# Optimization experiments

Measured on AMD Instinct MI355X. Metric: run time of the kernel, lower is better.

## Reference

```python
import jax, jax.numpy as jnp
import numpy as np

NEG_SLOPE = 0.2
EPS = 1e-16

N_NODES = 50000
N_EDGES = 1600000
IN_CH = 256
HID = 16
HEADS = 2


def setup_inputs() -> dict:
    key = jax.random.key(0)
    ks = jax.random.split(key, 12)
    s = lambda k, shape, scale=0.1: jax.random.normal(k, shape, dtype=jnp.float32) * scale
    x = jax.random.normal(ks[0], (N_NODES, IN_CH), dtype=jnp.float32)
    edge_index = jax.random.randint(ks[1], (2, N_EDGES), 0, N_NODES, dtype=jnp.int64)
    return {
        "x": x,
        "edge_index": edge_index,
        "W1": s(ks[2], (IN_CH, HEADS * HID)),
        "att_src1": s(ks[3], (HEADS, HID)),
        "att_dst1": s(ks[4], (HEADS, HID)),
        "b1": jnp.zeros((HEADS * HID,), jnp.float32),
        "W2": s(ks[5], (HEADS * HID, HID)),
        "att_src2": s(ks[6], (1, HID)),
        "att_dst2": s(ks[7], (1, HID)),
        "b2": jnp.zeros((HID,), jnp.float32),
        "Wm1": s(ks[8], (2 * HID, HID)),
        "bm1": jnp.zeros((HID,), jnp.float32),
        "Wm2": s(ks[9], (HID, 1)),
        "bm2": jnp.zeros((1,), jnp.float32),
    }


def gat_conv(x, src, dst, W, att_src, att_dst, bias, heads, out_ch, concat):
    # x: [N, F] -> h: [N, H, C]
    n = x.shape[0]
    h = (x @ W).reshape(n, heads, out_ch)
    # per-node attention logits [N, H]
    a_src = jnp.sum(h * att_src, axis=-1)
    a_dst = jnp.sum(h * att_dst, axis=-1)
    # per-edge logits: message j (src) -> i (dst); softmax grouped by dst
    e = a_src[src] + a_dst[dst]                      # [E, H]
    e = jax.nn.leaky_relu(e, NEG_SLOPE)
    e_max = jax.ops.segment_max(e, dst, num_segments=n)
    e_exp = jnp.exp(e - e_max[dst])
    denom = jax.ops.segment_sum(e_exp, dst, num_segments=n)
    alpha = e_exp / (denom[dst] + EPS)               # [E, H]
    msg = alpha[:, :, None] * h[src]                 # [E, H, C]
    out = jax.ops.segment_sum(msg, dst, num_segments=n)  # [N, H, C]
    out = out.reshape(n, heads * out_ch) if concat else out.mean(axis=1)
    return out + bias


def reference(x, edge_index, W1, att_src1, att_dst1, b1,
              W2, att_src2, att_dst2, b2, Wm1, bm1, Wm2, bm2):
    src, dst = edge_index[0], edge_index[1]
    # eval mode: feature/attention dropout are identity
    h = gat_conv(x, src, dst, W1, att_src1, att_dst1, b1, HEADS, HID, concat=True)
    h = jax.nn.elu(h)
    h = gat_conv(h, src, dst, W2, att_src2, att_dst2, b2, 1, HID, concat=False)
    # edge MLP on gathered (src, dst) node pairs
    ef = jnp.concatenate([h[src], h[dst]], axis=-1)  # [E, 2*HID]
    ef = jax.nn.relu(ef @ Wm1 + bm1)
    flow = (ef @ Wm2 + bm2).squeeze(-1)              # [E]
    return jax.nn.relu(flow)
```

## Files before the change

### kernel.cpp

```cpp
#include <hip/hip_runtime.h>
#include <hip/hip_bf16.h>
#include <hip/hip_fp16.h>

#define N_NODES 50000
#define N_EDGES 1600000
#define IN_CH 256
#define NEG_SLOPE 0.2f
#define EPS_F 1e-16f
#define CNT_PAD 16
#define CAP 128
#define NBK 196
#define CAPB 10240
#define PCHUNK 3125
#define KTILE 64
#define XS_PITCH (KTILE + 4)

__device__ __forceinline__ float lrelu(float x) {
    return x > 0.f ? x : NEG_SLOPE * x;
}

__device__ __forceinline__ float2 h2f(unsigned int w) {
    __half2 h;
    *reinterpret_cast<unsigned int*>(&h) = w;
    return __half22float2(h);
}

__device__ __forceinline__ unsigned int f2h2(float a, float b) {
    __half2 h = __floats2half2_rn(a, b);
    return *reinterpret_cast<unsigned int*>(&h);
}

__device__ __forceinline__ int detect_i64(const int* __restrict__ ei) {
    const int lane = threadIdx.x & 63;
    const unsigned long long b = __ballot(ei[2 * lane + 1] != 0);
    return b == 0ull ? 1 : 0;
}

__device__ __forceinline__ int ld_src(const int* ei, int f, int e) {
    return f ? ei[2 * (size_t)e] : ei[e];
}
__device__ __forceinline__ int ld_dst(const int* ei, int f, int e) {
    return f ? ei[2 * (size_t)N_EDGES + 2 * (size_t)e]
             : ei[(size_t)N_EDGES + e];
}

__global__ __launch_bounds__(1024) void k_part(const int* __restrict__ ei,
                                               int* __restrict__ gcnt,
                                               int2* __restrict__ bseg)
{
    __shared__ int hist[NBK];
    __shared__ int cur[NBK];
    const int t = threadIdx.x;
    const int f = detect_i64(ei);
    for (int j = t; j < NBK; j += 1024) hist[j] = 0;
    __syncthreads();
    const int e0 = blockIdx.x * PCHUNK;
    const int e1 = min(e0 + PCHUNK, N_EDGES);
    for (int e = e0 + t; e < e1; e += 1024)
        atomicAdd(&hist[ld_dst(ei, f, e) >> 8], 1);
    __syncthreads();
    for (int j = t; j < NBK; j += 1024)
        cur[j] = j * CAPB + atomicAdd(&gcnt[j], hist[j]);
    __syncthreads();
    for (int e = e0 + t; e < e1; e += 1024) {
        const int s = ld_src(ei, f, e);
        const int d = ld_dst(ei, f, e);
        const int bk = d >> 8;
        const int pos = atomicAdd(&cur[bk], 1);
        if (pos - bk * CAPB < CAPB) bseg[pos] = make_int2(s, d);
    }
}

__global__ __launch_bounds__(1024) void k_sub(const int* __restrict__ gcnt,
                                              const int2* __restrict__ bseg,
                                              int* __restrict__ cnt,
                                              int* __restrict__ csr_src)
{
    __shared__ int cur[256];
    const int b = blockIdx.x;
    const int t = threadIdx.x;
    if (t < 256) cur[t] = 0;
    __syncthreads();
    const int count = min(gcnt[b], CAPB);
    const int2* seg = bseg + (size_t)b * CAPB;
    for (int i = t; i < count; i += 1024) {
        const int2 e = seg[i];
        const int slot = atomicAdd(&cur[e.y & 255], 1);
        if (slot < CAP) csr_src[((size_t)e.y << 7) + slot] = e.x;
    }
    __syncthreads();
    if (t < 256) {
        const int n = b * 256 + t;
        if (n < N_NODES) cnt[(size_t)n * CNT_PAD] = min(cur[t], CAP);
    }
}

__global__ __launch_bounds__(256) void k1_gemm1(
    const float* __restrict__ x, const float* __restrict__ W1,
    const float* __restrict__ att_src1, const float* __restrict__ att_dst1,
    __half* __restrict__ h1, float* __restrict__ a_src1, float* __restrict__ a_dst1)
{
    __shared__ float w1s[IN_CH * 32];
    __shared__ float xs[64 * XS_PITCH];
    __shared__ float attss[32], attds[32];
    const int t = threadIdx.x;
    for (int i = t; i < IN_CH * 32; i += 256) w1s[i] = W1[i];
    if (t < 32) { attss[t] = att_src1[t]; attds[t] = att_dst1[t]; }
    const int row0 = blockIdx.x * 64;
    const int colq = t & 7, c4 = colq * 4;
    const int rp = t >> 3;
    const int r0 = rp * 2, r1 = r0 + 1;
    float4 a0 = make_float4(0.f, 0.f, 0.f, 0.f);
    float4 a1 = make_float4(0.f, 0.f, 0.f, 0.f);
    for (int kb = 0; kb < IN_CH; kb += KTILE) {
        __syncthreads();
        #pragma unroll
        for (int i = 0; i < 4; ++i) {
            const int idx = t + 256 * i;
            const int r = idx >> 4, p = idx & 15;
            const int row = row0 + r;
            float4 vv = make_float4(0.f, 0.f, 0.f, 0.f);
            if (row < N_NODES)
                vv = *(const float4*)(x + (size_t)row * IN_CH + kb + p * 4);
            *(float4*)(&xs[r * XS_PITCH + p * 4]) = vv;
        }
        __syncthreads();
        #pragma unroll 8
        for (int kt = 0; kt < KTILE; ++kt) {
            const float xv0 = xs[r0 * XS_PITCH + kt];
            const float xv1 = xs[r1 * XS_PITCH + kt];
            const float4 wv = *(const float4*)(&w1s[(kb + kt) * 32 + c4]);
            a0.x += xv0 * wv.x; a0.y += xv0 * wv.y;
            a0.z += xv0 * wv.z; a0.w += xv0 * wv.w;
            a1.x += xv1 * wv.x; a1.y += xv1 * wv.y;
            a1.z += xv1 * wv.z; a1.w += xv1 * wv.w;
        }
    }
    const int row_a = row0 + r0, row_b = row0 + r1;
    if (row_a < N_NODES) {
        uint2 p; p.x = f2h2(a0.x, a0.y); p.y = f2h2(a0.z, a0.w);
        *(uint2*)(h1 + (size_t)row_a * 32 + c4) = p;
    }
    if (row_b < N_NODES) {
        uint2 p; p.x = f2h2(a1.x, a1.y); p.y = f2h2(a1.z, a1.w);
        *(uint2*)(h1 + (size_t)row_b * 32 + c4) = p;
    }
    float sa0 = a0.x * attss[c4] + a0.y * attss[c4 + 1]
              + a0.z * attss[c4 + 2] + a0.w * attss[c4 + 3];
    float sd0 = a0.x * attds[c4] + a0.y * attds[c4 + 1]
              + a0.z * attds[c4 + 2] + a0.w * attds[c4 + 3];
    float sa1 = a1.x * attss[c4] + a1.y * attss[c4 + 1]
              + a1.z * attss[c4 + 2] + a1.w * attss[c4 + 3];
    float sd1 = a1.x * attds[c4] + a1.y * attds[c4 + 1]
              + a1.z * attds[c4 + 2] + a1.w * attds[c4 + 3];
    sa0 += __shfl_xor(sa0, 1); sa0 += __shfl_xor(sa0, 2);
    sd0 += __shfl_xor(sd0, 1); sd0 += __shfl_xor(sd0, 2);
    sa1 += __shfl_xor(sa1, 1); sa1 += __shfl_xor(sa1, 2);
    sd1 += __shfl_xor(sd1, 1); sd1 += __shfl_xor(sd1, 2);
    const int head = colq >> 2;
    if ((colq & 3) == 0) {
        if (row_a < N_NODES) {
            a_src1[row_a * 2 + head] = sa0;
            a_dst1[row_a * 2 + head] = sd0;
        }
        if (row_b < N_NODES) {
            a_src1[row_b * 2 + head] = sa1;
            a_dst1[row_b * 2 + head] = sd1;
        }
    }
}

__global__ __launch_bounds__(256) void k_agg1f(
    const int* __restrict__ cnt, const int* __restrict__ csr_src,
    const float* __restrict__ a_src1, const float* __restrict__ a_dst1,
    const __half* __restrict__ h1,
    const float* __restrict__ b1, const float* __restrict__ W2,
    const float* __restrict__ att_src2, const float* __restrict__ att_dst2,
    __half* __restrict__ h2, float* __restrict__ a_src2, float* __restrict__ a_dst2)
{
    __shared__ float w2s[32 * 16];
    __shared__ float b1s[32], as2[16], ad2[16];
    __shared__ float act_s[4][32];
    const int t = threadIdx.x;
    for (int i = t; i < 512; i += 256) w2s[i] = W2[i];
    if (t < 32) b1s[t] = b1[t];
    if (t < 16) { as2[t] = att_src2[t]; ad2[t] = att_dst2[t]; }

    const int wid = (blockIdx.x * 256 + t) >> 6;
    const int lane = t & 63;
    const int wv = t >> 6;
    const int active = (wid < N_NODES);
    const int len = active ? min(cnt[(size_t)wid * CNT_PAD], CAP) : 0;
    const int beg = wid << 7, end = beg + len;
    float2 ad = make_float2(0.f, 0.f);
    if (active) ad = *(const float2*)(a_dst1 + 2 * (size_t)wid);
    const int slot = lane >> 4, chp = lane & 15;
    const int head = chp >> 3;
    const float adh = head ? ad.y : ad.x;
    const int rep = ((chp & 7) == 0);
    const unsigned int* __restrict__ h1u = (const unsigned int*)h1;
    float accx = 0.f, accy = 0.f, sw = 0.f;
    int i = beg + slot;
    for (; i + 28 < end; i += 32) {
        int s[8]; float a[8]; unsigned int hw[8]; float w[8];
        #pragma unroll
        for (int j = 0; j < 8; ++j) s[j] = csr_src[i + 4 * j];
        #pragma unroll
        for (int j = 0; j < 8; ++j) a[j] = a_src1[2 * (size_t)s[j] + head];
        #pragma unroll
        for (int j = 0; j < 8; ++j) hw[j] = h1u[(size_t)s[j] * 16 + chp];
        #pragma unroll
        for (int j = 0; j < 8; ++j) w[j] = __expf(lrelu(a[j] + adh));
        float wsum = 0.f;
        #pragma unroll
        for (int j = 0; j < 8; ++j) {
            const float2 hf = h2f(hw[j]);
            wsum += w[j];
            accx += w[j] * hf.x; accy += w[j] * hf.y;
        }
        if (rep) sw += wsum;
    }
    for (; i + 12 < end; i += 16) {
        int s[4]; float a[4]; unsigned int hw[4]; float w[4];
        #pragma unroll
        for (int j = 0; j < 4; ++j) s[j] = csr_src[i + 4 * j];
        #pragma unroll
        for (int j = 0; j < 4; ++j) a[j] = a_src1[2 * (size_t)s[j] + head];
        #pragma unroll
        for (int j = 0; j < 4; ++j) hw[j] = h1u[(size_t)s[j] * 16 + chp];
        #pragma unroll
        for (int j = 0; j < 4; ++j) w[j] = __expf(lrelu(a[j] + adh));
        float wsum = 0.f;
        #pragma unroll
        for (int j = 0; j < 4; ++j) {
            const float2 hf = h2f(hw[j]);
            wsum += w[j];
            accx += w[j] * hf.x; accy += w[j] * hf.y;
        }
        if (rep) sw += wsum;
    }
    for (; i < end; i += 4) {
        const int s = csr_src[i];
        const float w = __expf(lrelu(a_src1[2 * (size_t)s + head] + adh));
        if (rep) sw += w;
        const float2 hf = h2f(h1u[(size_t)s * 16 + chp]);
        accx += w * hf.x; accy += w * hf.y;
    }
    sw += __shfl_xor(sw, 16); sw += __shfl_xor(sw, 32);
    const float swh = __shfl(sw, head << 3);
    accx += __shfl_xor(accx, 16); accx += __shfl_xor(accx, 32);
    accy += __shfl_xor(accy, 16); accy += __shfl_xor(accy, 32);
    const float inv = 1.f / (swh + EPS_F);
    if (lane < 16) {
        float ax = accx * inv + b1s[2 * chp];
        float ay = accy * inv + b1s[2 * chp + 1];
        ax = ax > 0.f ? ax : expm1f(ax);
        ay = ay > 0.f ? ay : expm1f(ay);
        act_s[wv][2 * chp] = ax;
        act_s[wv][2 * chp + 1] = ay;
    }
    __syncthreads();
    const int j = lane & 15;
    float acc2 = 0.f;
    #pragma unroll
    for (int k = 0; k < 32; ++k) acc2 += act_s[wv][k] * w2s[k * 16 + j];
    if (lane < 16 && active) h2[(size_t)wid * 16 + j] = __float2half(acc2);
    float sa = acc2 * as2[j], sd = acc2 * ad2[j];
    sa += __shfl_xor(sa, 1); sa += __shfl_xor(sa, 2);
    sa += __shfl_xor(sa, 4); sa += __shfl_xor(sa, 8);
    sd += __shfl_xor(sd, 1); sd += __shfl_xor(sd, 2);
    sd += __shfl_xor(sd, 4); sd += __shfl_xor(sd, 8);
    if (lane == 0 && active) { a_src2[wid] = sa; a_dst2[wid] = sd; }
}

__global__ __launch_bounds__(256) void k_agg2f(
    const int* __restrict__ cnt, const int* __restrict__ csr_src,
    const float* __restrict__ a_src2, const float* __restrict__ a_dst2,
    const __half* __restrict__ h2,
    const float* __restrict__ b2, const float* __restrict__ Wm1,
    const float* __restrict__ bm1,
    __half* __restrict__ u, __half* __restrict__ v)
{
    __shared__ float wa[16 * 16], wb[16 * 16];
    __shared__ float b2s[16], bm1s[16];
    __shared__ float act_s[4][16];
    const int t = threadIdx.x;
    if (t < 256) { wa[t] = Wm1[t]; wb[t] = Wm1[256 + t]; }
    if (t < 16) { b2s[t] = b2[t]; bm1s[t] = bm1[t]; }

    const int wid = (blockIdx.x * 256 + t) >> 6;
    const int lane = t & 63;
    const int wv = t >> 6;
    const int active = (wid < N_NODES);
    const int len = active ? min(cnt[(size_t)wid * CNT_PAD], CAP) : 0;
    const int beg = wid << 7, end = beg + len;
    const float ad = active ? a_dst2[wid] : 0.f;
    const int slot = lane >> 3, chp = lane & 7;
    const int rep = (chp == 0);
    const unsigned int* __restrict__ h2u = (const unsigned int*)h2;
    float accx = 0.f, accy = 0.f, sw = 0.f;
    int i = beg + slot;
    for (; i + 24 < end; i += 32) {
        int s[4]; float a[4]; unsigned int hw[4]; float w[4];
        #pragma unroll
        for (int j = 0; j < 4; ++j) s[j] = csr_src[i + 8 * j];
        #pragma unroll
        for (int j = 0; j < 4; ++j) a[j] = a_src2[s[j]];
        #pragma unroll
        for (int j = 0; j < 4; ++j) hw[j] = h2u[(size_t)s[j] * 8 + chp];
        #pragma unroll
        for (int j = 0; j < 4; ++j) w[j] = __expf(lrelu(a[j] + ad));
        float wsum = 0.f;
        #pragma unroll
        for (int j = 0; j < 4; ++j) {
            const float2 hf = h2f(hw[j]);
            wsum += w[j];
            accx += w[j] * hf.x; accy += w[j] * hf.y;
        }
        if (rep) sw += wsum;
    }
    for (; i < end; i += 8) {
        const int s = csr_src[i];
        const float w = __expf(lrelu(a_src2[s] + ad));
        if (rep) sw += w;
        const float2 hf = h2f(h2u[(size_t)s * 8 + chp]);
        accx += w * hf.x; accy += w * hf.y;
    }
    sw += __shfl_xor(sw, 8); sw += __shfl_xor(sw, 16); sw += __shfl_xor(sw, 32);
    const float swt = __shfl(sw, 0);
    accx += __shfl_xor(accx, 8); accx += __shfl_xor(accx, 16); accx += __shfl_xor(accx, 32);
    accy += __shfl_xor(accy, 8); accy += __shfl_xor(accy, 16); accy += __shfl_xor(accy, 32);
    const float inv = 1.f / (swt + EPS_F);
    if (lane < 8) {
        float2 o;
        o.x = accx * inv + b2s[2 * chp];
        o.y = accy * inv + b2s[2 * chp + 1];
        *(float2*)(&act_s[wv][2 * chp]) = o;
    }
    __syncthreads();
    const int c = lane & 15;
    float su = bm1s[c], sv = 0.f;
    #pragma unroll
    for (int k = 0; k < 16; ++k) {
        const float a = act_s[wv][k];
        su += a * wa[k * 16 + c];
        sv += a * wb[k * 16 + c];
    }
    if (lane < 16 && active) {
        u[(size_t)wid * 16 + c] = __float2half(su);
        v[(size_t)wid * 16 + c] = __float2half(sv);
    }
}

__global__ __launch_bounds__(256) void k7_lite(
    const int* __restrict__ ei,
    const __half* __restrict__ u, const __half* __restrict__ v,
    const float* __restrict__ Wm2, const float* __restrict__ bm2,
    float* __restrict__ out)
{
    __shared__ float wm2s[16];
    __shared__ float bm2s;
    const int t = threadIdx.x;
    const int f = detect_i64(ei);
    if (t < 16) wm2s[t] = Wm2[t];
    if (t == 0) bm2s = bm2[0];
    __syncthreads();
    const int e = blockIdx.x * 256 + t;
    if (e >= N_EDGES) return;
    const int s = ld_src(ei, f, e);
    const int d = ld_dst(ei, f, e);
    const uint4* up = (const uint4*)(u + (size_t)s * 16);
    const uint4* vp = (const uint4*)(v + (size_t)d * 16);
    const uint4 ua = up[0], ub = up[1];
    const uint4 va = vp[0], vb = vp[1];
    float fl = bm2s;
    unsigned int uw[8] = {ua.x, ua.y, ua.z, ua.w, ub.x, ub.y, ub.z, ub.w};
    unsigned int vw[8] = {va.x, va.y, va.z, va.w, vb.x, vb.y, vb.z, vb.w};
    #pragma unroll
    for (int i = 0; i < 8; ++i) {
        const float2 a = h2f(uw[i]);
        const float2 b = h2f(vw[i]);
        fl += fmaxf(a.x + b.x, 0.f) * wm2s[2 * i];
        fl += fmaxf(a.y + b.y, 0.f) * wm2s[2 * i + 1];
    }
    out[e] = fmaxf(fl, 0.f);
}

extern "C" void kernel_launch(void* const* d_in, const int* in_sizes, int n_in,
                              void* d_out, int out_size, void* d_ws, size_t ws_size,
                              hipStream_t stream)
{
    const float* x        = (const float*)d_in[0];
    const int*   ei       = (const int*)d_in[1];
    const float* W1       = (const float*)d_in[2];
    const float* att_src1 = (const float*)d_in[3];
    const float* att_dst1 = (const float*)d_in[4];
    const float* b1       = (const float*)d_in[5];
    const float* W2       = (const float*)d_in[6];
    const float* att_src2 = (const float*)d_in[7];
    const float* att_dst2 = (const float*)d_in[8];
    const float* b2       = (const float*)d_in[9];
    const float* Wm1      = (const float*)d_in[10];
    const float* bm1      = (const float*)d_in[11];
    const float* Wm2      = (const float*)d_in[12];
    const float* bm2      = (const float*)d_in[13];

    float* ws = (float*)d_ws;
    size_t off = 0;
    __half* h1 = (__half*)(ws + off); off += 16 * (size_t)N_NODES;
    float* a_src1 = ws + off; off += 2  * (size_t)N_NODES;
    float* a_dst1 = ws + off; off += 2  * (size_t)N_NODES;
    float* out1_dead = ws + off; off += 32 * (size_t)N_NODES;
    __half* h2 = (__half*)(ws + off); off += 16 * (size_t)N_NODES;
    float* a_src2 = ws + off; off += 1  * (size_t)N_NODES;
    float* a_dst2 = ws + off; off += 1  * (size_t)N_NODES;
    float* out2_dead = ws + off; off += 16 * (size_t)N_NODES;
    __half* u = (__half*)(ws + off); off += 8 * (size_t)N_NODES;
    __half* v = (__half*)(ws + off); off += 8 * (size_t)N_NODES;
    int* cnt     = (int*)(ws + off); off += (size_t)N_NODES * CNT_PAD;
    int* csr_src = (int*)(ws + off); off += (size_t)N_NODES * CAP;
    int* gcnt    = (int*)(ws + off); off += 256;
    int* flag    = (int*)(ws + off); off += 64;
    (void)out1_dead; (void)out2_dead; (void)flag;
    int2* bseg = (int2*)ws;

    hipMemsetAsync(gcnt, 0, 256 * sizeof(int), stream);
    k_part<<<(N_EDGES + PCHUNK - 1) / PCHUNK, 1024, 0, stream>>>(ei, gcnt, bseg);
    k_sub<<<NBK, 1024, 0, stream>>>(gcnt, bseg, cnt, csr_src);

    k1_gemm1<<<(N_NODES + 63) / 64, 256, 0, stream>>>(
        x, W1, att_src1, att_dst1, h1, a_src1, a_dst1);
    k_agg1f<<<(N_NODES + 3) / 4, 256, 0, stream>>>(
        cnt, csr_src, a_src1, a_dst1, h1, b1, W2, att_src2, att_dst2,
        h2, a_src2, a_dst2);
    k_agg2f<<<(N_NODES + 3) / 4, 256, 0, stream>>>(
        cnt, csr_src, a_src2, a_dst2, h2, b2, Wm1, bm1, u, v);
    k7_lite<<<(N_EDGES + 255) / 256, 256, 0, stream>>>(
        ei, u, v, Wm2, bm2, (float*)d_out);
}
```

Measured before the change: 259.3 us.

## Compute edge weights once per edge and broadcast via shuffles in GAT aggregation

The two neighbor-aggregation kernels now have each lane load one CSR source index and compute one attention weight, then broadcast indices and weights to the channel lanes with wave shuffles. Before, every channel lane reloaded csr_src and a_src and recomputed exp redundantly. The partition kernel also keeps the src/dst values it loaded in registers between the histogram and scatter passes, so edge_index is read once instead of twice. This adds many shuffle instructions and loses the multi-edge unrolled loads that were in flight together, which may reduce memory-level parallelism for the feature gathers.

```diff
diff --git a/kernel.cpp b/kernel.cpp
--- a/kernel.cpp
+++ b/kernel.cpp
@@ -56,18 +56,26 @@
     __syncthreads();
     const int e0 = blockIdx.x * PCHUNK;
     const int e1 = min(e0 + PCHUNK, N_EDGES);
-    for (int e = e0 + t; e < e1; e += 1024)
-        atomicAdd(&hist[ld_dst(ei, f, e) >> 8], 1);
+    int es[4], ed[4];
+    int ne = 0;
+    #pragma unroll
+    for (int q = 0; q < 4; ++q) {
+        const int e = e0 + t + 1024 * q;
+        if (e < e1) {
+            es[ne] = ld_src(ei, f, e);
+            ed[ne] = ld_dst(ei, f, e);
+            ++ne;
+        }
+    }
+    for (int q = 0; q < ne; ++q) atomicAdd(&hist[ed[q] >> 8], 1);
     __syncthreads();
     for (int j = t; j < NBK; j += 1024)
         cur[j] = j * CAPB + atomicAdd(&gcnt[j], hist[j]);
     __syncthreads();
-    for (int e = e0 + t; e < e1; e += 1024) {
-        const int s = ld_src(ei, f, e);
-        const int d = ld_dst(ei, f, e);
-        const int bk = d >> 8;
+    for (int q = 0; q < ne; ++q) {
+        const int bk = ed[q] >> 8;
         const int pos = atomicAdd(&cur[bk], 1);
-        if (pos - bk * CAPB < CAPB) bseg[pos] = make_int2(s, d);
+        if (pos - bk * CAPB < CAPB) bseg[pos] = make_int2(es[q], ed[q]);
     }
 }
 
@@ -194,60 +202,36 @@
     const int beg = wid << 7, end = beg + len;
     float2 ad = make_float2(0.f, 0.f);
     if (active) ad = *(const float2*)(a_dst1 + 2 * (size_t)wid);
+
+    const int e_off = lane >> 1;
+    const int hh = lane & 1;
+    const float adh_a = hh ? ad.y : ad.x;
     const int slot = lane >> 4, chp = lane & 15;
     const int head = chp >> 3;
-    const float adh = head ? ad.y : ad.x;
-    const int rep = ((chp & 7) == 0);
+
     const unsigned int* __restrict__ h1u = (const unsigned int*)h1;
     float accx = 0.f, accy = 0.f, sw = 0.f;
-    int i = beg + slot;
-    for (; i + 28 < end; i += 32) {
-        int s[8]; float a[8]; unsigned int hw[8]; float w[8];
-        #pragma unroll
-        for (int j = 0; j < 8; ++j) s[j] = csr_src[i + 4 * j];
-        #pragma unroll
-        for (int j = 0; j < 8; ++j) a[j] = a_src1[2 * (size_t)s[j] + head];
-        #pragma unroll
-        for (int j = 0; j < 8; ++j) hw[j] = h1u[(size_t)s[j] * 16 + chp];
-        #pragma unroll
-        for (int j = 0; j < 8; ++j) w[j] = __expf(lrelu(a[j] + adh));
-        float wsum = 0.f;
+    for (int i0 = beg; i0 < end; i0 += 32) {
+        const int el = i0 + e_off;
+        int s_a = 0; float w_a = 0.f;
+        if (el < end) {
+            s_a = csr_src[el];
+            const float av = a_src1[2 * (size_t)s_a + hh];
+            w_a = __expf(lrelu(av + adh_a));
+        }
+        sw += w_a;
         #pragma unroll
         for (int j = 0; j < 8; ++j) {
-            const float2 hf = h2f(hw[j]);
-            wsum += w[j];
-            accx += w[j] * hf.x; accy += w[j] * hf.y;
-        }
-        if (rep) sw += wsum;
-    }
-    for (; i + 12 < end; i += 16) {
-        int s[4]; float a[4]; unsigned int hw[4]; float w[4];
-        #pragma unroll
-        for (int j = 0; j < 4; ++j) s[j] = csr_src[i + 4 * j];
-        #pragma unroll
-        for (int j = 0; j < 4; ++j) a[j] = a_src1[2 * (size_t)s[j] + head];
-        #pragma unroll
-        for (int j = 0; j < 4; ++j) hw[j] = h1u[(size_t)s[j] * 16 + chp];
-        #pragma unroll
-        for (int j = 0; j < 4; ++j) w[j] = __expf(lrelu(a[j] + adh));
-        float wsum = 0.f;
-        #pragma unroll
-        for (int j = 0; j < 4; ++j) {
-            const float2 hf = h2f(hw[j]);
-            wsum += w[j];
-            accx += w[j] * hf.x; accy += w[j] * hf.y;
-        }
-        if (rep) sw += wsum;
-    }
-    for (; i < end; i += 4) {
-        const int s = csr_src[i];
-        const float w = __expf(lrelu(a_src1[2 * (size_t)s + head] + adh));
-        if (rep) sw += w;
-        const float2 hf = h2f(h1u[(size_t)s * 16 + chp]);
-        accx += w * hf.x; accy += w * hf.y;
-    }
-    sw += __shfl_xor(sw, 16); sw += __shfl_xor(sw, 32);
-    const float swh = __shfl(sw, head << 3);
+            const int sl = (slot * 8 + j) * 2;
+            const int s_j = __shfl(s_a, sl);
+            const float w_j = __shfl(w_a, sl + head);
+            const float2 hf = h2f(h1u[(size_t)s_j * 16 + chp]);
+            accx += w_j * hf.x; accy += w_j * hf.y;
+        }
+    }
+    sw += __shfl_xor(sw, 2); sw += __shfl_xor(sw, 4);
+    sw += __shfl_xor(sw, 8); sw += __shfl_xor(sw, 16); sw += __shfl_xor(sw, 32);
+    const float swh = __shfl(sw, head);
     accx += __shfl_xor(accx, 16); accx += __shfl_xor(accx, 32);
     accy += __shfl_xor(accy, 16); accy += __shfl_xor(accy, 32);
     const float inv = 1.f / (swh + EPS_F);
@@ -296,41 +280,30 @@
     const int beg = wid << 7, end = beg + len;
     const float ad = active ? a_dst2[wid] : 0.f;
     const int slot = lane >> 3, chp = lane & 7;
-    const int rep = (chp == 0);
     const unsigned int* __restrict__ h2u = (const unsigned int*)h2;
     float accx = 0.f, accy = 0.f, sw = 0.f;
-    int i = beg + slot;
-    for (; i + 24 < end; i += 32) {
-        int s[4]; float a[4]; unsigned int hw[4]; float w[4];
+    for (int i0 = beg; i0 < end; i0 += 64) {
+        const int el = i0 + lane;
+        int s_a = 0; float w_a = 0.f;
+        if (el < end) {
+            s_a = csr_src[el];
+            w_a = __expf(lrelu(a_src2[s_a] + ad));
+        }
+        sw += w_a;
         #pragma unroll
-        for (int j = 0; j < 4; ++j) s[j] = csr_src[i + 8 * j];
-        #pragma unroll
-        for (int j = 0; j < 4; ++j) a[j] = a_src2[s[j]];
-        #pragma unroll
-        for (int j = 0; j < 4; ++j) hw[j] = h2u[(size_t)s[j] * 8 + chp];
-        #pragma unroll
-        for (int j = 0; j < 4; ++j) w[j] = __expf(lrelu(a[j] + ad));
-        float wsum = 0.f;
-        #pragma unroll
-        for (int j = 0; j < 4; ++j) {
-            const float2 hf = h2f(hw[j]);
-            wsum += w[j];
-            accx += w[j] * hf.x; accy += w[j] * hf.y;
-        }
-        if (rep) sw += wsum;
-    }
-    for (; i < end; i += 8) {
-        const int s = csr_src[i];
-        const float w = __expf(lrelu(a_src2[s] + ad));
-        if (rep) sw += w;
-        const float2 hf = h2f(h2u[(size_t)s * 8 + chp]);
-        accx += w * hf.x; accy += w * hf.y;
-    }
+        for (int j = 0; j < 8; ++j) {
+            const int sl = slot * 8 + j;
+            const int s_j = __shfl(s_a, sl);
+            const float w_j = __shfl(w_a, sl);
+            const float2 hf = h2f(h2u[(size_t)s_j * 8 + chp]);
+            accx += w_j * hf.x; accy += w_j * hf.y;
+        }
+    }
+    sw += __shfl_xor(sw, 1); sw += __shfl_xor(sw, 2); sw += __shfl_xor(sw, 4);
     sw += __shfl_xor(sw, 8); sw += __shfl_xor(sw, 16); sw += __shfl_xor(sw, 32);
-    const float swt = __shfl(sw, 0);
     accx += __shfl_xor(accx, 8); accx += __shfl_xor(accx, 16); accx += __shfl_xor(accx, 32);
     accy += __shfl_xor(accy, 8); accy += __shfl_xor(accy, 16); accy += __shfl_xor(accy, 32);
-    const float inv = 1.f / (swt + EPS_F);
+    const float inv = 1.f / (sw + EPS_F);
     if (lane < 8) {
         float2 o;
         o.x = accx * inv + b2s[2 * chp];
```

Result: no change. 259.1 us (-0.1%).

## Replace two-pass bucketed CSR build with direct global-atomic slot insertion

Applied to the files above, without the earlier changes.

Removes the two-kernel partition (block histogram into 196 buckets, then a per-bucket sub-sort through LDS atomics) and builds the padded CSR in one kernel. That kernel does a global atomicAdd on each destination's padded counter and writes the source into that slot. This drops one launch and the intermediate bseg round trip. In exchange it issues 1.6M scattered global atomics, and a memset now has to clear the padded count array. Slot order inside a node becomes nondeterministic, which can change float summation order.

```diff
diff --git a/kernel.cpp b/kernel.cpp
--- a/kernel.cpp
+++ b/kernel.cpp
@@ -9,9 +9,6 @@
 #define EPS_F 1e-16f
 #define CNT_PAD 16
 #define CAP 128
-#define NBK 196
-#define CAPB 10240
-#define PCHUNK 3125
 #define KTILE 64
 #define XS_PITCH (KTILE + 4)
 
@@ -44,55 +41,17 @@
              : ei[(size_t)N_EDGES + e];
 }
 
-__global__ __launch_bounds__(1024) void k_part(const int* __restrict__ ei,
-                                               int* __restrict__ gcnt,
-                                               int2* __restrict__ bseg)
-{
-    __shared__ int hist[NBK];
-    __shared__ int cur[NBK];
-    const int t = threadIdx.x;
+__global__ __launch_bounds__(256) void k_build(const int* __restrict__ ei,
+                                               int* __restrict__ cnt,
+                                               int* __restrict__ csr_src)
+{
     const int f = detect_i64(ei);
-    for (int j = t; j < NBK; j += 1024) hist[j] = 0;
-    __syncthreads();
-    const int e0 = blockIdx.x * PCHUNK;
-    const int e1 = min(e0 + PCHUNK, N_EDGES);
-    for (int e = e0 + t; e < e1; e += 1024)
-        atomicAdd(&hist[ld_dst(ei, f, e) >> 8], 1);
-    __syncthreads();
-    for (int j = t; j < NBK; j += 1024)
-        cur[j] = j * CAPB + atomicAdd(&gcnt[j], hist[j]);
-    __syncthreads();
-    for (int e = e0 + t; e < e1; e += 1024) {
-        const int s = ld_src(ei, f, e);
-        const int d = ld_dst(ei, f, e);
-        const int bk = d >> 8;
-        const int pos = atomicAdd(&cur[bk], 1);
-        if (pos - bk * CAPB < CAPB) bseg[pos] = make_int2(s, d);
-    }
-}
-
-__global__ __launch_bounds__(1024) void k_sub(const int* __restrict__ gcnt,
-                                              const int2* __restrict__ bseg,
-                                              int* __restrict__ cnt,
-                                              int* __restrict__ csr_src)
-{
-    __shared__ int cur[256];
-    const int b = blockIdx.x;
-    const int t = threadIdx.x;
-    if (t < 256) cur[t] = 0;
-    __syncthreads();
-    const int count = min(gcnt[b], CAPB);
-    const int2* seg = bseg + (size_t)b * CAPB;
-    for (int i = t; i < count; i += 1024) {
-        const int2 e = seg[i];
-        const int slot = atomicAdd(&cur[e.y & 255], 1);
-        if (slot < CAP) csr_src[((size_t)e.y << 7) + slot] = e.x;
-    }
-    __syncthreads();
-    if (t < 256) {
-        const int n = b * 256 + t;
-        if (n < N_NODES) cnt[(size_t)n * CNT_PAD] = min(cur[t], CAP);
-    }
+    const int e = blockIdx.x * 256 + threadIdx.x;
+    if (e >= N_EDGES) return;
+    const int s = ld_src(ei, f, e);
+    const int d = ld_dst(ei, f, e);
+    const int pos = atomicAdd(&cnt[(size_t)d * CNT_PAD], 1);
+    if (pos < CAP) csr_src[((size_t)d << 7) + pos] = s;
 }
 
 __global__ __launch_bounds__(256) void k1_gemm1(
@@ -410,23 +369,19 @@
     __half* h1 = (__half*)(ws + off); off += 16 * (size_t)N_NODES;
     float* a_src1 = ws + off; off += 2  * (size_t)N_NODES;
     float* a_dst1 = ws + off; off += 2  * (size_t)N_NODES;
-    float* out1_dead = ws + off; off += 32 * (size_t)N_NODES;
+    float* spare1 = ws + off; off += 32 * (size_t)N_NODES;
     __half* h2 = (__half*)(ws + off); off += 16 * (size_t)N_NODES;
     float* a_src2 = ws + off; off += 1  * (size_t)N_NODES;
     float* a_dst2 = ws + off; off += 1  * (size_t)N_NODES;
-    float* out2_dead = ws + off; off += 16 * (size_t)N_NODES;
+    float* spare2 = ws + off; off += 16 * (size_t)N_NODES;
     __half* u = (__half*)(ws + off); off += 8 * (size_t)N_NODES;
     __half* v = (__half*)(ws + off); off += 8 * (size_t)N_NODES;
     int* cnt     = (int*)(ws + off); off += (size_t)N_NODES * CNT_PAD;
     int* csr_src = (int*)(ws + off); off += (size_t)N_NODES * CAP;
-    int* gcnt    = (int*)(ws + off); off += 256;
-    int* flag    = (int*)(ws + off); off += 64;
-    (void)out1_dead; (void)out2_dead; (void)flag;
-    int2* bseg = (int2*)ws;
-
-    hipMemsetAsync(gcnt, 0, 256 * sizeof(int), stream);
-    k_part<<<(N_EDGES + PCHUNK - 1) / PCHUNK, 1024, 0, stream>>>(ei, gcnt, bseg);
-    k_sub<<<NBK, 1024, 0, stream>>>(gcnt, bseg, cnt, csr_src);
+    (void)spare1; (void)spare2;
+
+    hipMemsetAsync(cnt, 0, (size_t)N_NODES * CNT_PAD * sizeof(int), stream);
+    k_build<<<(N_EDGES + 255) / 256, 256, 0, stream>>>(ei, cnt, csr_src);
 
     k1_gemm1<<<(N_NODES + 63) / 64, 256, 0, stream>>>(
         x, W1, att_src1, att_dst1, h1, a_src1, a_dst1);
```

Result: slower. 340.9 us (+31.5%).

## Precompute layer-1 attention weights into CSR records during bucket scatter

Applied to the files above, without the earlier changes.

Reorders the launches so the first GEMM runs before CSR construction. The sub-bucket scatter can then compute both heads' exp(leaky_relu) layer-1 attention weights and store them next to the source index in 16-byte records. The layer-1 aggregation reads these records in place of gathering a_src1 and evaluating exp per edge per lane. The partition kernel also keeps its src/dst loads in registers so edge_index is read once, not twice. In exchange CSR storage grows fourfold, so the layer-2 aggregation reads 16-byte records just to get the index, and k_sub now does random gathers of a_src1.

```diff
diff --git a/kernel.cpp b/kernel.cpp
--- a/kernel.cpp
+++ b/kernel.cpp
@@ -56,25 +56,35 @@
     __syncthreads();
     const int e0 = blockIdx.x * PCHUNK;
     const int e1 = min(e0 + PCHUNK, N_EDGES);
-    for (int e = e0 + t; e < e1; e += 1024)
-        atomicAdd(&hist[ld_dst(ei, f, e) >> 8], 1);
+    int es[4], ed[4];
+    int ne = 0;
+    #pragma unroll
+    for (int q = 0; q < 4; ++q) {
+        const int e = e0 + t + 1024 * q;
+        if (e < e1) {
+            es[ne] = ld_src(ei, f, e);
+            ed[ne] = ld_dst(ei, f, e);
+            ++ne;
+        }
+    }
+    for (int q = 0; q < ne; ++q) atomicAdd(&hist[ed[q] >> 8], 1);
     __syncthreads();
     for (int j = t; j < NBK; j += 1024)
         cur[j] = j * CAPB + atomicAdd(&gcnt[j], hist[j]);
     __syncthreads();
-    for (int e = e0 + t; e < e1; e += 1024) {
-        const int s = ld_src(ei, f, e);
-        const int d = ld_dst(ei, f, e);
-        const int bk = d >> 8;
+    for (int q = 0; q < ne; ++q) {
+        const int bk = ed[q] >> 8;
         const int pos = atomicAdd(&cur[bk], 1);
-        if (pos - bk * CAPB < CAPB) bseg[pos] = make_int2(s, d);
+        if (pos - bk * CAPB < CAPB) bseg[pos] = make_int2(es[q], ed[q]);
     }
 }
 
 __global__ __launch_bounds__(1024) void k_sub(const int* __restrict__ gcnt,
                                               const int2* __restrict__ bseg,
+                                              const float* __restrict__ a_src1,
+                                              const float* __restrict__ a_dst1,
                                               int* __restrict__ cnt,
-                                              int* __restrict__ csr_src)
+                                              int4* __restrict__ csr_rec)
 {
     __shared__ int cur[256];
     const int b = blockIdx.x;
@@ -86,7 +96,18 @@
     for (int i = t; i < count; i += 1024) {
         const int2 e = seg[i];
         const int slot = atomicAdd(&cur[e.y & 255], 1);
-        if (slot < CAP) csr_src[((size_t)e.y << 7) + slot] = e.x;
+        if (slot < CAP) {
+            const float2 as = *(const float2*)(a_src1 + 2 * (size_t)e.x);
+            const float2 ad = *(const float2*)(a_dst1 + 2 * (size_t)e.y);
+            const float w0 = __expf(lrelu(as.x + ad.x));
+            const float w1 = __expf(lrelu(as.y + ad.y));
+            int4 r;
+            r.x = e.x;
+            r.y = __float_as_int(w0);
+            r.z = __float_as_int(w1);
+            r.w = 0;
+            csr_rec[((size_t)e.y << 7) + slot] = r;
+        }
     }
     __syncthreads();
     if (t < 256) {
@@ -171,8 +192,8 @@
 }
 
 __global__ __launch_bounds__(256) void k_agg1f(
-    const int* __restrict__ cnt, const int* __restrict__ csr_src,
-    const float* __restrict__ a_src1, const float* __restrict__ a_dst1,
+    const int* __restrict__ cnt, const int4* __restrict__ csr_rec,
+    const float* __restrict__ a_dst1,
     const __half* __restrict__ h1,
     const float* __restrict__ b1, const float* __restrict__ W2,
     const float* __restrict__ att_src2, const float* __restrict__ att_dst2,
@@ -192,58 +213,49 @@
     const int active = (wid < N_NODES);
     const int len = active ? min(cnt[(size_t)wid * CNT_PAD], CAP) : 0;
     const int beg = wid << 7, end = beg + len;
-    float2 ad = make_float2(0.f, 0.f);
-    if (active) ad = *(const float2*)(a_dst1 + 2 * (size_t)wid);
     const int slot = lane >> 4, chp = lane & 15;
     const int head = chp >> 3;
-    const float adh = head ? ad.y : ad.x;
     const int rep = ((chp & 7) == 0);
     const unsigned int* __restrict__ h1u = (const unsigned int*)h1;
     float accx = 0.f, accy = 0.f, sw = 0.f;
     int i = beg + slot;
     for (; i + 28 < end; i += 32) {
-        int s[8]; float a[8]; unsigned int hw[8]; float w[8];
-        #pragma unroll
-        for (int j = 0; j < 8; ++j) s[j] = csr_src[i + 4 * j];
-        #pragma unroll
-        for (int j = 0; j < 8; ++j) a[j] = a_src1[2 * (size_t)s[j] + head];
-        #pragma unroll
-        for (int j = 0; j < 8; ++j) hw[j] = h1u[(size_t)s[j] * 16 + chp];
-        #pragma unroll
-        for (int j = 0; j < 8; ++j) w[j] = __expf(lrelu(a[j] + adh));
+        int4 r[8]; unsigned int hw[8];
+        #pragma unroll
+        for (int j = 0; j < 8; ++j) r[j] = csr_rec[i + 4 * j];
+        #pragma unroll
+        for (int j = 0; j < 8; ++j) hw[j] = h1u[(size_t)r[j].x * 16 + chp];
         float wsum = 0.f;
         #pragma unroll
         for (int j = 0; j < 8; ++j) {
+            const float w = __int_as_float(head ? r[j].z : r[j].y);
             const float2 hf = h2f(hw[j]);
-            wsum += w[j];
-            accx += w[j] * hf.x; accy += w[j] * hf.y;
+            wsum += w;
+            accx += w * hf.x; accy += w * hf.y;
         }
         if (rep) sw += wsum;
     }
     for (; i + 12 < end; i += 16) {
-        int s[4]; float a[4]; unsigned int hw[4]; float w[4];
-        #pragma unroll
-        for (int j = 0; j < 4; ++j) s[j] = csr_src[i + 4 * j];
-        #pragma unroll
-        for (int j = 0; j < 4; ++j) a[j] = a_src1[2 * (size_t)s[j] + head];
-        #pragma unroll
-        for (int j = 0; j < 4; ++j) hw[j] = h1u[(size_t)s[j] * 16 + chp];
-        #pragma unroll
-        for (int j = 0; j < 4; ++j) w[j] = __expf(lrelu(a[j] + adh));
+        int4 r[4]; unsigned int hw[4];
+        #pragma unroll
+        for (int j = 0; j < 4; ++j) r[j] = csr_rec[i + 4 * j];
+        #pragma unroll
+        for (int j = 0; j < 4; ++j) hw[j] = h1u[(size_t)r[j].x * 16 + chp];
         float wsum = 0.f;
         #pragma unroll
         for (int j = 0; j < 4; ++j) {
+            const float w = __int_as_float(head ? r[j].z : r[j].y);
             const float2 hf = h2f(hw[j]);
-            wsum += w[j];
-            accx += w[j] * hf.x; accy += w[j] * hf.y;
+            wsum += w;
+            accx += w * hf.x; accy += w * hf.y;
         }
         if (rep) sw += wsum;
     }
     for (; i < end; i += 4) {
-        const int s = csr_src[i];
-        const float w = __expf(lrelu(a_src1[2 * (size_t)s + head] + adh));
+        const int4 r = csr_rec[i];
+        const float w = __int_as_float(head ? r.z : r.y);
         if (rep) sw += w;
-        const float2 hf = h2f(h1u[(size_t)s * 16 + chp]);
+        const float2 hf = h2f(h1u[(size_t)r.x * 16 + chp]);
         accx += w * hf.x; accy += w * hf.y;
     }
     sw += __shfl_xor(sw, 16); sw += __shfl_xor(sw, 32);
@@ -274,7 +286,7 @@
 }
 
 __global__ __launch_bounds__(256) void k_agg2f(
-    const int* __restrict__ cnt, const int* __restrict__ csr_src,
+    const int* __restrict__ cnt, const int4* __restrict__ csr_rec,
     const float* __restrict__ a_src2, const float* __restrict__ a_dst2,
     const __half* __restrict__ h2,
     const float* __restrict__ b2, const float* __restrict__ Wm1,
@@ -303,7 +315,7 @@
     for (; i + 24 < end; i += 32) {
         int s[4]; float a[4]; unsigned int hw[4]; float w[4];
         #pragma unroll
-        for (int j = 0; j < 4; ++j) s[j] = csr_src[i + 8 * j];
+        for (int j = 0; j < 4; ++j) s[j] = csr_rec[i + 8 * j].x;
         #pragma unroll
         for (int j = 0; j < 4; ++j) a[j] = a_src2[s[j]];
         #pragma unroll
@@ -320,7 +332,7 @@
         if (rep) sw += wsum;
     }
     for (; i < end; i += 8) {
-        const int s = csr_src[i];
+        const int s = csr_rec[i].x;
         const float w = __expf(lrelu(a_src2[s] + ad));
         if (rep) sw += w;
         const float2 hf = h2f(h2u[(size_t)s * 8 + chp]);
@@ -410,31 +422,27 @@
     __half* h1 = (__half*)(ws + off); off += 16 * (size_t)N_NODES;
     float* a_src1 = ws + off; off += 2  * (size_t)N_NODES;
     float* a_dst1 = ws + off; off += 2  * (size_t)N_NODES;
-    float* out1_dead = ws + off; off += 32 * (size_t)N_NODES;
-    __half* h2 = (__half*)(ws + off); off += 16 * (size_t)N_NODES;
+    __half* h2 = (__half*)(ws + off); off += 8 * (size_t)N_NODES;
     float* a_src2 = ws + off; off += 1  * (size_t)N_NODES;
     float* a_dst2 = ws + off; off += 1  * (size_t)N_NODES;
-    float* out2_dead = ws + off; off += 16 * (size_t)N_NODES;
     __half* u = (__half*)(ws + off); off += 8 * (size_t)N_NODES;
     __half* v = (__half*)(ws + off); off += 8 * (size_t)N_NODES;
-    int* cnt     = (int*)(ws + off); off += (size_t)N_NODES * CNT_PAD;
-    int* csr_src = (int*)(ws + off); off += (size_t)N_NODES * CAP;
-    int* gcnt    = (int*)(ws + off); off += 256;
-    int* flag    = (int*)(ws + off); off += 64;
-    (void)out1_dead; (void)out2_dead; (void)flag;
-    int2* bseg = (int2*)ws;
+    int* cnt      = (int*)(ws + off);  off += (size_t)N_NODES * CNT_PAD;
+    int4* csr_rec = (int4*)(ws + off); off += (size_t)N_NODES * CAP * 4;
+    int2* bseg    = (int2*)(ws + off); off += (size_t)NBK * CAPB * 2;
+    int* gcnt     = (int*)(ws + off);  off += 256;
 
     hipMemsetAsync(gcnt, 0, 256 * sizeof(int), stream);
-    k_part<<<(N_EDGES + PCHUNK - 1) / PCHUNK, 1024, 0, stream>>>(ei, gcnt, bseg);
-    k_sub<<<NBK, 1024, 0, stream>>>(gcnt, bseg, cnt, csr_src);
-
     k1_gemm1<<<(N_NODES + 63) / 64, 256, 0, stream>>>(
         x, W1, att_src1, att_dst1, h1, a_src1, a_dst1);
+    k_part<<<(N_EDGES + PCHUNK - 1) / PCHUNK, 1024, 0, stream>>>(ei, gcnt, bseg);
+    k_sub<<<NBK, 1024, 0, stream>>>(gcnt, bseg, a_src1, a_dst1, cnt, csr_rec);
+
     k_agg1f<<<(N_NODES + 3) / 4, 256, 0, stream>>>(
-        cnt, csr_src, a_src1, a_dst1, h1, b1, W2, att_src2, att_dst2,
+        cnt, csr_rec, a_dst1, h1, b1, W2, att_src2, att_dst2,
         h2, a_src2, a_dst2);
     k_agg2f<<<(N_NODES + 3) / 4, 256, 0, stream>>>(
-        cnt, csr_src, a_src2, a_dst2, h2, b2, Wm1, bm1, u, v);
+        cnt, csr_rec, a_src2, a_dst2, h2, b2, Wm1, bm1, u, v);
     k7_lite<<<(N_EDGES + 255) / 256, 256, 0, stream>>>(
         ei, u, v, Wm2, bm2, (float*)d_out);
 }
```

Result: slower. 281.8 us (+8.7%).
